# Kernel tuning notes

Measured on AMD Instinct MI355X. Metric: run time of the kernel, lower is better.

Reference implementation:

```python
import jax, jax.numpy as jnp
import numpy as np

THRESHOLD = 0.004  # graph_threshold from init_kwargs
EPS = 1e-12


def setup_inputs() -> dict:
    key = jax.random.key(0)
    kf, kw = jax.random.split(key)
    features = jax.random.normal(kf, (8192, 128), dtype=jnp.float32)
    weight = jax.random.normal(kw, (128, 128), dtype=jnp.float32)
    return {"features": features, "weight": weight}


def reference(features, weight):
    # Pairwise state fidelity: squared dot product of row-normalized vectors.
    n = features.shape[0]
    xn = features / (jnp.linalg.norm(features, axis=1, keepdims=True) + EPS)
    fid = (xn @ xn.T) ** 2  # [N, N]
    # Edge weight 1.0 where fid >= threshold (secondary=None); no self-loops.
    adj = (fid >= THRESHOLD).astype(features.dtype)
    adj = adj * (1.0 - jnp.eye(n, dtype=features.dtype))
    aggregated = adj @ features  # [N, F]
    # relu(W @ agg.T).T == relu(agg @ W.T)
    return jax.nn.relu(aggregated @ weight.T)
```

## Files before the change

### kernel.cpp

```cpp
#include <hip/hip_runtime.h>
#include <math.h>

#define NROWS 8192
#define NF    128
#define THRF  0.004f
#define BM    128
#define BN    64
#define QN    2048
#define NITER 32

typedef _Float16 f16;
typedef __attribute__((ext_vector_type(8))) _Float16 f16x8;
typedef __attribute__((ext_vector_type(4))) float f32x4;

#define MFMA16F(a, b, c) __builtin_amdgcn_mfma_f32_16x16x32_f16(a, b, c, 0, 0, 0)

#define RH_OFF 0
#define RL_OFF 32768
#define TB_OFF 65536
#define PB_OFF 98304
#define IJ_OFF 114688
#define SM_BYTES 115200

typedef __attribute__((address_space(1))) const unsigned int g_u32;
typedef __attribute__((address_space(3))) unsigned int l_u32;

__device__ __forceinline__ void gload16(const void* g, void* l) {
    __builtin_amdgcn_global_load_lds((g_u32*)g, (l_u32*)l, 16, 0, 0);
}

__device__ __forceinline__ unsigned short f16bits(f16 x) {
    return __builtin_bit_cast(unsigned short, x);
}

__global__ __launch_bounds__(256) void prep_k(const float* __restrict__ X,
                                              float* __restrict__ inv_norm,
                                              unsigned short* __restrict__ Xh,
                                              unsigned short* __restrict__ Xl,
                                              unsigned short* __restrict__ XhT) {
    __shared__ unsigned short sT[64][136];
    const int t  = threadIdx.x;
    const int jb = blockIdx.x * 64;
    const int row = t >> 2, c0 = (t & 3) * 32;
    const int grow = jb + row;

    float v[32];
    {
        const float* src = X + (size_t)grow * NF + c0;
        #pragma unroll
        for (int k = 0; k < 8; ++k) {
            f32x4 e = *reinterpret_cast<const f32x4*>(src + 4 * k);
            v[4 * k]     = e[0]; v[4 * k + 1] = e[1];
            v[4 * k + 2] = e[2]; v[4 * k + 3] = e[3];
        }
    }
    float ss = 0.f;
    #pragma unroll
    for (int k = 0; k < 32; ++k) ss += v[k] * v[k];
    ss += __shfl_xor(ss, 1);
    ss += __shfl_xor(ss, 2);
    if ((t & 3) == 0) inv_norm[grow] = 1.0f / (sqrtf(ss) + 1e-12f);

    #pragma unroll
    for (int k = 0; k < 4; ++k) {
        unsigned hw[4], lw[4];
        #pragma unroll
        for (int p = 0; p < 4; ++p) {
            float a = v[8 * k + 2 * p], b = v[8 * k + 2 * p + 1];
            f16 ha = (f16)a, hb = (f16)b;
            f16 la = (f16)((a - (float)ha) * 2048.0f);
            f16 lb = (f16)((b - (float)hb) * 2048.0f);
            hw[p] = (unsigned)f16bits(ha) | ((unsigned)f16bits(hb) << 16);
            lw[p] = (unsigned)f16bits(la) | ((unsigned)f16bits(lb) << 16);
        }
        uint4 h4 = {hw[0], hw[1], hw[2], hw[3]};
        uint4 l4 = {lw[0], lw[1], lw[2], lw[3]};
        *reinterpret_cast<uint4*>(Xh + (size_t)grow * NF + c0 + 8 * k) = h4;
        *reinterpret_cast<uint4*>(Xl + (size_t)grow * NF + c0 + 8 * k) = l4;
        unsigned* sp = reinterpret_cast<unsigned*>(&sT[row][c0 + 8 * k]);
        sp[0] = hw[0]; sp[1] = hw[1]; sp[2] = hw[2]; sp[3] = hw[3];
    }
    __syncthreads();
    {
        int f = t >> 1, qh = t & 1;
        unsigned um[16];
        #pragma unroll
        for (int m = 0; m < 16; ++m) {
            int j = 32 * qh + 2 * m;
            um[m] = (unsigned)sT[j][f] | ((unsigned)sT[j + 1][f] << 16);
        }
        unsigned* dst = reinterpret_cast<unsigned*>(XhT + (size_t)f * NROWS + jb + 32 * qh);
        #pragma unroll
        for (int m = 0; m < 16; ++m) dst[m] = um[m];
    }
}

__device__ __forceinline__ void issue_tiles(const unsigned short* __restrict__ Xh,
                                            const unsigned short* __restrict__ Xl,
                                            const unsigned short* __restrict__ XhT,
                                            char* SM, int w, int l, int jwin, int buf) {
    const int r16 = l >> 4, c16 = l & 15;
    #pragma unroll
    for (int u = 0; u < 2; ++u) {
        int jloc = 8 * w + 4 * u + r16;
        size_t src = (size_t)(jwin + jloc) * NF + ((c16 ^ (jloc & 15)) << 3);
        gload16(Xh + src, SM + RH_OFF + buf * 16384 + (8 * w + 4 * u) * 256);
        gload16(Xl + src, SM + RL_OFF + buf * 16384 + (8 * w + 4 * u) * 256);
    }
    const int r8 = l >> 3, c8 = l & 7;
    #pragma unroll
    for (int u = 0; u < 2; ++u) {
        int floc = 16 * w + 8 * u + r8;
        const unsigned short* src = XhT + (size_t)floc * NROWS + jwin + ((c8 ^ (floc & 7)) << 3);
        gload16(src, SM + TB_OFF + buf * 16384 + (16 * w + 8 * u) * 128);
    }
}

__global__ __launch_bounds__(512, 2) void fused_k(const unsigned short* __restrict__ Xh,
                                                  const unsigned short* __restrict__ Xl,
                                                  const unsigned short* __restrict__ XhT,
                                                  const float* __restrict__ inv_norm,
                                                  float* __restrict__ out) {
    __shared__ __align__(16) char SM[SM_BYTES];
    const int t = threadIdx.x;
    const int w = t >> 6, l = t & 63, l15 = l & 15, h = l >> 4;
    const int im2 = w >> 1;
    const int jn2 = w & 1;
    const int bid   = blockIdx.x;
    const int ibase = (bid >> 2) * BM;
    const int qbase = (bid & 3) * QN;

    f16x8 aH[2][4], aL[2][4];
    #pragma unroll
    for (int is = 0; is < 2; ++is) {
        const size_t ro = (size_t)(ibase + 32 * im2 + 16 * is + l15) * NF;
        #pragma unroll
        for (int ks = 0; ks < 4; ++ks) {
            aH[is][ks] = *reinterpret_cast<const f16x8*>(Xh + ro + 32 * ks + 8 * h);
            aL[is][ks] = *reinterpret_cast<const f16x8*>(Xl + ro + 32 * ks + 8 * h);
        }
    }
    float invI2[8];
    #pragma unroll
    for (int is = 0; is < 2; ++is)
        #pragma unroll
        for (int q = 0; q < 4; ++q) {
            float x = inv_norm[ibase + 32 * im2 + 16 * is + 4 * h + q];
            invI2[is * 4 + q] = x * x;
        }

    issue_tiles(Xh, Xl, XhT, SM, w, l, qbase, 0);
    if (t < BN) { float x = inv_norm[qbase + t]; ((float*)(SM + IJ_OFF))[t] = x * x; }

    f32x4 agg[2][4];
    #pragma unroll
    for (int is = 0; is < 2; ++is)
        #pragma unroll
        for (int fs = 0; fs < 4; ++fs)
            #pragma unroll
            for (int q = 0; q < 4; ++q) agg[is][fs][q] = 0.f;

    for (int it = 0; it < NITER; ++it) {
        const int buf  = it & 1;
        const int jwin = qbase + it * BN;
        __syncthreads();
        if (it + 1 < NITER) {
            issue_tiles(Xh, Xl, XhT, SM, w, l, jwin + BN, buf ^ 1);
            if (t < BN) {
                float x = inv_norm[jwin + BN + t];
                ((float*)(SM + IJ_OFF))[(buf ^ 1) * BN + t] = x * x;
            }
        }
        const char* rh = SM + RH_OFF + buf * 16384;
        const char* rl = SM + RL_OFF + buf * 16384;
        f32x4 Shi[2][2], Slo[2][2];
        #pragma unroll
        for (int js = 0; js < 2; ++js)
            #pragma unroll
            for (int is = 0; is < 2; ++is)
                #pragma unroll
                for (int q = 0; q < 4; ++q) { Shi[js][is][q] = 0.f; Slo[js][is][q] = 0.f; }
        __builtin_amdgcn_s_setprio(1);
        #pragma unroll
        for (int ks = 0; ks < 4; ++ks) {
            #pragma unroll
            for (int js = 0; js < 2; ++js) {
                int jl = 32 * jn2 + 16 * js + l15;
                int boff = jl * 256 + (((4 * ks + h) ^ (jl & 15)) << 4);
                f16x8 bh = *reinterpret_cast<const f16x8*>(rh + boff);
                f16x8 bl = *reinterpret_cast<const f16x8*>(rl + boff);
                #pragma unroll
                for (int is = 0; is < 2; ++is) {
                    Shi[js][is] = MFMA16F(aH[is][ks], bh, Shi[js][is]);
                    Slo[js][is] = MFMA16F(aL[is][ks], bh, Slo[js][is]);
                    Slo[js][is] = MFMA16F(aH[is][ks], bl, Slo[js][is]);
                }
            }
        }
        __builtin_amdgcn_s_setprio(0);

        #pragma unroll
        for (int js = 0; js < 2; ++js) {
            int jc = 32 * jn2 + 16 * js + l15;
            float ij2 = ((const float*)(SM + IJ_OFF))[buf * BN + jc];
            #pragma unroll
            for (int is = 0; is < 2; ++is) {
                int di = (jwin + jc) - (ibase + 32 * im2 + 16 * is + 4 * h);
                #pragma unroll
                for (int q = 0; q < 4; ++q) {
                    float vv = Shi[js][is][q] + Slo[js][is][q] * (1.0f / 2048.0f);
                    float t2 = vv * vv * invI2[is * 4 + q] * ij2;
                    bool p = (t2 >= THRF) && (di != q);
                    int il = 32 * im2 + 16 * is + 4 * h + q;
                    int pb = il * 128 + ((jc * 2) ^ ((il & 7) << 4));
                    *reinterpret_cast<unsigned short*>(SM + PB_OFF + pb) =
                        p ? (unsigned short)0x3C00 : (unsigned short)0;
                }
            }
        }
        asm volatile("s_waitcnt lgkmcnt(0)\n\ts_barrier" ::: "memory");

        const char* tbp = SM + TB_OFF + buf * 16384;
        __builtin_amdgcn_s_setprio(1);
        #pragma unroll
        for (int kj = 0; kj < 2; ++kj) {
            f16x8 pa[2];
            #pragma unroll
            for (int is = 0; is < 2; ++is) {
                int ir = 32 * im2 + 16 * is + l15;
                pa[is] = *reinterpret_cast<const f16x8*>(
                    SM + PB_OFF + ir * 128 + ((64 * kj + 16 * h) ^ ((ir & 7) << 4)));
            }
            #pragma unroll
            for (int fs = 0; fs < 4; ++fs) {
                int f = 64 * jn2 + 16 * fs + l15;
                f16x8 bt = *reinterpret_cast<const f16x8*>(
                    tbp + f * 128 + ((64 * kj + 16 * h) ^ ((f & 7) << 4)));
                agg[0][fs] = MFMA16F(pa[0], bt, agg[0][fs]);
                agg[1][fs] = MFMA16F(pa[1], bt, agg[1][fs]);
            }
        }
        __builtin_amdgcn_s_setprio(0);
    }

    #pragma unroll
    for (int is = 0; is < 2; ++is)
        #pragma unroll
        for (int fs = 0; fs < 4; ++fs) {
            int col = 64 * jn2 + 16 * fs + l15;
            #pragma unroll
            for (int q = 0; q < 4; ++q) {
                int row = ibase + 32 * im2 + 16 * is + 4 * h + q;
                atomicAdd(&out[(size_t)row * NF + col], agg[is][fs][q]);
            }
        }
}

__global__ __launch_bounds__(256) void combine_k(const float* __restrict__ Wm,
                                                 float* __restrict__ out) {
    __shared__ float sW[NF * NF];
    __shared__ float sSum[32][132];
    const int t = threadIdx.x;
    const size_t base = (size_t)blockIdx.x * 32 * NF;
    #pragma unroll
    for (int k = 0; k < 16; ++k) {
        int u4 = t + 256 * k;
        reinterpret_cast<f32x4*>(sW)[u4] = reinterpret_cast<const f32x4*>(Wm)[u4];
    }
    #pragma unroll
    for (int k = 0; k < 4; ++k) {
        int u4 = t + 256 * k;
        f32x4 v = reinterpret_cast<const f32x4*>(out + base)[u4];
        *reinterpret_cast<f32x4*>(&sSum[u4 >> 5][(4 * u4) & 127]) = v;
    }
    __syncthreads();
    const int r = t & 31, og = t >> 5;
    float acc[16];
    #pragma unroll
    for (int oi = 0; oi < 16; ++oi) acc[oi] = 0.f;
    #pragma unroll 8
    for (int k4 = 0; k4 < 32; ++k4) {
        f32x4 a4 = *reinterpret_cast<const f32x4*>(&sSum[r][4 * k4]);
        #pragma unroll
        for (int oi = 0; oi < 16; ++oi) {
            f32x4 w4 = *reinterpret_cast<const f32x4*>(&sW[(og * 16 + oi) * NF + 4 * k4]);
            acc[oi] += a4[0] * w4[0] + a4[1] * w4[1] + a4[2] * w4[2] + a4[3] * w4[3];
        }
    }
    #pragma unroll
    for (int o4 = 0; o4 < 4; ++o4) {
        f32x4 v4;
        #pragma unroll
        for (int e = 0; e < 4; ++e) {
            float v = acc[o4 * 4 + e];
            v4[e] = v > 0.f ? v : 0.f;
        }
        *reinterpret_cast<f32x4*>(out + base + r * NF + og * 16 + o4 * 4) = v4;
    }
}

extern "C" void kernel_launch(void* const* d_in, const int* in_sizes, int n_in,
                              void* d_out, int out_size, void* d_ws, size_t ws_size,
                              hipStream_t stream) {
    const float* feat = (const float*)d_in[0];
    const float* Wm   = (const float*)d_in[1];
    float* out        = (float*)d_out;

    char* ws = (char*)d_ws;
    unsigned short* Xh  = (unsigned short*)(ws);
    unsigned short* Xl  = (unsigned short*)(ws + (2u << 20));
    unsigned short* XhT = (unsigned short*)(ws + (4u << 20));
    float* inv_norm     = (float*)(ws + (6u << 20));

    hipMemsetAsync(out, 0, (size_t)out_size * sizeof(float), stream);
    prep_k<<<NROWS / 64, 256, 0, stream>>>(feat, inv_norm, Xh, Xl, XhT);
    fused_k<<<256, 512, 0, stream>>>(Xh, Xl, XhT, inv_norm, out);
    combine_k<<<NROWS / 32, 256, 0, stream>>>(Wm, out);
}
```

Before: 107.9 us.

## Remap warp tiling to 2x4 layout and replace memset with zero kernel

Warps are now arranged as 2 along rows by 4 along columns. Each warp covers 64 rows and 16 j-columns in the fidelity GEMM, so it loads each B fragment once and reuses it across 4 row subtiles, and it covers 32 feature columns in the aggregation GEMM. This cuts the LDS B reads in the first GEMM but doubles the A-fragment registers (aH/aL become 4x4), which raises register pressure at 2 blocks per CU. The hipMemsetAsync on the output is replaced by a small vectorized zeroing kernel to avoid memset overhead.

After: 126.1 us. +16.8%, slower.

```diff
diff --git a/kernel.cpp b/kernel.cpp
--- a/kernel.cpp
+++ b/kernel.cpp
@@ -31,6 +31,13 @@
 
 __device__ __forceinline__ unsigned short f16bits(f16 x) {
     return __builtin_bit_cast(unsigned short, x);
+}
+
+__global__ __launch_bounds__(256) void zero_k(float* __restrict__ out) {
+    int idx = blockIdx.x * 512 + threadIdx.x;
+    f32x4 z = {0.f, 0.f, 0.f, 0.f};
+    reinterpret_cast<f32x4*>(out)[idx]       = z;
+    reinterpret_cast<f32x4*>(out)[idx + 256] = z;
 }
 
 __global__ __launch_bounds__(256) void prep_k(const float* __restrict__ X,
@@ -124,41 +131,43 @@
     __shared__ __align__(16) char SM[SM_BYTES];
     const int t = threadIdx.x;
     const int w = t >> 6, l = t & 63, l15 = l & 15, h = l >> 4;
-    const int im2 = w >> 1;
-    const int jn2 = w & 1;
+    const int iw = w & 1;
+    const int jw = w >> 1;
     const int bid   = blockIdx.x;
     const int ibase = (bid >> 2) * BM;
     const int qbase = (bid & 3) * QN;
 
-    f16x8 aH[2][4], aL[2][4];
-    #pragma unroll
-    for (int is = 0; is < 2; ++is) {
-        const size_t ro = (size_t)(ibase + 32 * im2 + 16 * is + l15) * NF;
+    f16x8 aH[4][4], aL[4][4];
+    #pragma unroll
+    for (int is = 0; is < 4; ++is) {
+        const size_t ro = (size_t)(ibase + 64 * iw + 16 * is + l15) * NF;
         #pragma unroll
         for (int ks = 0; ks < 4; ++ks) {
             aH[is][ks] = *reinterpret_cast<const f16x8*>(Xh + ro + 32 * ks + 8 * h);
             aL[is][ks] = *reinterpret_cast<const f16x8*>(Xl + ro + 32 * ks + 8 * h);
         }
     }
-    float invI2[8];
-    #pragma unroll
-    for (int is = 0; is < 2; ++is)
+    float invI2[16];
+    #pragma unroll
+    for (int is = 0; is < 4; ++is)
         #pragma unroll
         for (int q = 0; q < 4; ++q) {
-            float x = inv_norm[ibase + 32 * im2 + 16 * is + 4 * h + q];
+            float x = inv_norm[ibase + 64 * iw + 16 * is + 4 * h + q];
             invI2[is * 4 + q] = x * x;
         }
 
     issue_tiles(Xh, Xl, XhT, SM, w, l, qbase, 0);
     if (t < BN) { float x = inv_norm[qbase + t]; ((float*)(SM + IJ_OFF))[t] = x * x; }
 
-    f32x4 agg[2][4];
-    #pragma unroll
-    for (int is = 0; is < 2; ++is)
-        #pragma unroll
-        for (int fs = 0; fs < 4; ++fs)
-            #pragma unroll
-            for (int q = 0; q < 4; ++q) agg[is][fs][q] = 0.f;
+    f32x4 agg[4][2];
+    #pragma unroll
+    for (int is = 0; is < 4; ++is)
+        #pragma unroll
+        for (int nf = 0; nf < 2; ++nf)
+            #pragma unroll
+            for (int q = 0; q < 4; ++q) agg[is][nf][q] = 0.f;
+
+    const int jl = 16 * jw + l15;
 
     for (int it = 0; it < NITER; ++it) {
         const int buf  = it & 1;
@@ -171,48 +180,42 @@
                 ((float*)(SM + IJ_OFF))[(buf ^ 1) * BN + t] = x * x;
             }
         }
-        const char* rh = SM + RH_OFF + buf * 16384;
-        const char* rl = SM + RL_OFF + buf * 16384;
-        f32x4 Shi[2][2], Slo[2][2];
-        #pragma unroll
-        for (int js = 0; js < 2; ++js)
-            #pragma unroll
-            for (int is = 0; is < 2; ++is)
-                #pragma unroll
-                for (int q = 0; q < 4; ++q) { Shi[js][is][q] = 0.f; Slo[js][is][q] = 0.f; }
+        const char* rh  = SM + RH_OFF + buf * 16384;
+        const char* rl  = SM + RL_OFF + buf * 16384;
+        const char* tbp = SM + TB_OFF + buf * 16384;
+
+        f32x4 Shi[4], Slo[4];
+        #pragma unroll
+        for (int is = 0; is < 4; ++is)
+            #pragma unroll
+            for (int q = 0; q < 4; ++q) { Shi[is][q] = 0.f; Slo[is][q] = 0.f; }
         __builtin_amdgcn_s_setprio(1);
         #pragma unroll
         for (int ks = 0; ks < 4; ++ks) {
-            #pragma unroll
-            for (int js = 0; js < 2; ++js) {
-                int jl = 32 * jn2 + 16 * js + l15;
-                int boff = jl * 256 + (((4 * ks + h) ^ (jl & 15)) << 4);
-                f16x8 bh = *reinterpret_cast<const f16x8*>(rh + boff);
-                f16x8 bl = *reinterpret_cast<const f16x8*>(rl + boff);
-                #pragma unroll
-                for (int is = 0; is < 2; ++is) {
-                    Shi[js][is] = MFMA16F(aH[is][ks], bh, Shi[js][is]);
-                    Slo[js][is] = MFMA16F(aL[is][ks], bh, Slo[js][is]);
-                    Slo[js][is] = MFMA16F(aH[is][ks], bl, Slo[js][is]);
-                }
+            int boff = jl * 256 + (((4 * ks + h) ^ (jl & 15)) << 4);
+            f16x8 bh = *reinterpret_cast<const f16x8*>(rh + boff);
+            f16x8 bl = *reinterpret_cast<const f16x8*>(rl + boff);
+            #pragma unroll
+            for (int is = 0; is < 4; ++is) {
+                Shi[is] = MFMA16F(aH[is][ks], bh, Shi[is]);
+                Slo[is] = MFMA16F(aL[is][ks], bh, Slo[is]);
+                Slo[is] = MFMA16F(aH[is][ks], bl, Slo[is]);
             }
         }
         __builtin_amdgcn_s_setprio(0);
 
-        #pragma unroll
-        for (int js = 0; js < 2; ++js) {
-            int jc = 32 * jn2 + 16 * js + l15;
-            float ij2 = ((const float*)(SM + IJ_OFF))[buf * BN + jc];
-            #pragma unroll
-            for (int is = 0; is < 2; ++is) {
-                int di = (jwin + jc) - (ibase + 32 * im2 + 16 * is + 4 * h);
+        {
+            float ij2 = ((const float*)(SM + IJ_OFF))[buf * BN + jl];
+            #pragma unroll
+            for (int is = 0; is < 4; ++is) {
+                int di = (jwin + jl) - (ibase + 64 * iw + 16 * is + 4 * h);
                 #pragma unroll
                 for (int q = 0; q < 4; ++q) {
-                    float vv = Shi[js][is][q] + Slo[js][is][q] * (1.0f / 2048.0f);
+                    float vv = Shi[is][q] + Slo[is][q] * (1.0f / 2048.0f);
                     float t2 = vv * vv * invI2[is * 4 + q] * ij2;
                     bool p = (t2 >= THRF) && (di != q);
-                    int il = 32 * im2 + 16 * is + 4 * h + q;
-                    int pb = il * 128 + ((jc * 2) ^ ((il & 7) << 4));
+                    int il = 64 * iw + 16 * is + 4 * h + q;
+                    int pb = il * 128 + ((jl * 2) ^ ((il & 7) << 4));
                     *reinterpret_cast<unsigned short*>(SM + PB_OFF + pb) =
                         p ? (unsigned short)0x3C00 : (unsigned short)0;
                 }
@@ -220,38 +223,37 @@
         }
         asm volatile("s_waitcnt lgkmcnt(0)\n\ts_barrier" ::: "memory");
 
-        const char* tbp = SM + TB_OFF + buf * 16384;
         __builtin_amdgcn_s_setprio(1);
         #pragma unroll
         for (int kj = 0; kj < 2; ++kj) {
-            f16x8 pa[2];
-            #pragma unroll
-            for (int is = 0; is < 2; ++is) {
-                int ir = 32 * im2 + 16 * is + l15;
-                pa[is] = *reinterpret_cast<const f16x8*>(
+            f16x8 bt[2];
+            #pragma unroll
+            for (int nf = 0; nf < 2; ++nf) {
+                int f = 32 * jw + 16 * nf + l15;
+                bt[nf] = *reinterpret_cast<const f16x8*>(
+                    tbp + f * 128 + ((64 * kj + 16 * h) ^ ((f & 7) << 4)));
+            }
+            #pragma unroll
+            for (int is = 0; is < 4; ++is) {
+                int ir = 64 * iw + 16 * is + l15;
+                f16x8 pa = *reinterpret_cast<const f16x8*>(
                     SM + PB_OFF + ir * 128 + ((64 * kj + 16 * h) ^ ((ir & 7) << 4)));
-            }
-            #pragma unroll
-            for (int fs = 0; fs < 4; ++fs) {
-                int f = 64 * jn2 + 16 * fs + l15;
-                f16x8 bt = *reinterpret_cast<const f16x8*>(
-                    tbp + f * 128 + ((64 * kj + 16 * h) ^ ((f & 7) << 4)));
-                agg[0][fs] = MFMA16F(pa[0], bt, agg[0][fs]);
-                agg[1][fs] = MFMA16F(pa[1], bt, agg[1][fs]);
+                agg[is][0] = MFMA16F(pa, bt[0], agg[is][0]);
+                agg[is][1] = MFMA16F(pa, bt[1], agg[is][1]);
             }
         }
         __builtin_amdgcn_s_setprio(0);
     }
 
     #pragma unroll
-    for (int is = 0; is < 2; ++is)
-        #pragma unroll
-        for (int fs = 0; fs < 4; ++fs) {
-            int col = 64 * jn2 + 16 * fs + l15;
+    for (int is = 0; is < 4; ++is)
+        #pragma unroll
+        for (int nf = 0; nf < 2; ++nf) {
+            int col = 32 * jw + 16 * nf + l15;
             #pragma unroll
             for (int q = 0; q < 4; ++q) {
-                int row = ibase + 32 * im2 + 16 * is + 4 * h + q;
-                atomicAdd(&out[(size_t)row * NF + col], agg[is][fs][q]);
+                int row = ibase + 64 * iw + 16 * is + 4 * h + q;
+                atomicAdd(&out[(size_t)row * NF + col], agg[is][nf][q]);
             }
         }
 }
@@ -312,7 +314,7 @@
     unsigned short* XhT = (unsigned short*)(ws + (4u << 20));
     float* inv_norm     = (float*)(ws + (6u << 20));
 
-    hipMemsetAsync(out, 0, (size_t)out_size * sizeof(float), stream);
+    zero_k<<<NROWS * NF / 2048, 256, 0, stream>>>(out);
     prep_k<<<NROWS / 64, 256, 0, stream>>>(feat, inv_norm, Xh, Xl, XhT);
     fused_k<<<256, 512, 0, stream>>>(Xh, Xl, XhT, inv_norm, out);
     combine_k<<<NROWS / 32, 256, 0, stream>>>(Wm, out);
```

## Halve column tile and split work over twice as many blocks for occupancy

Applied to the files above, without the earlier changes.

Shrinks the per-iteration column window from 64 to 32 and the per-block column range from 2048 to 1024, so the fused kernel launches 512 blocks with half the LDS and an occupancy hint of 4 blocks per CU. Tile loading, the swizzles and the predicate buffer layout are reworked for the smaller tiles. The aim is more resident waves and better latency hiding on 256 CUs, at the cost of twice as many global atomic adds to the output and more barriers per unit of work. It also replaces hipMemsetAsync with a small zeroing kernel.

Result: slower. 180.6 us (+67.3%).

```diff
diff --git a/kernel.cpp b/kernel.cpp
--- a/kernel.cpp
+++ b/kernel.cpp
@@ -5,8 +5,8 @@
 #define NF    128
 #define THRF  0.004f
 #define BM    128
-#define BN    64
-#define QN    2048
+#define BN    32
+#define QN    1024
 #define NITER 32
 
 typedef _Float16 f16;
@@ -16,11 +16,11 @@
 #define MFMA16F(a, b, c) __builtin_amdgcn_mfma_f32_16x16x32_f16(a, b, c, 0, 0, 0)
 
 #define RH_OFF 0
-#define RL_OFF 32768
-#define TB_OFF 65536
-#define PB_OFF 98304
-#define IJ_OFF 114688
-#define SM_BYTES 115200
+#define RL_OFF 16384
+#define TB_OFF 32768
+#define PB_OFF 49152
+#define IJ_OFF 57344
+#define SM_BYTES 57600
 
 typedef __attribute__((address_space(1))) const unsigned int g_u32;
 typedef __attribute__((address_space(3))) unsigned int l_u32;
@@ -31,6 +31,13 @@
 
 __device__ __forceinline__ unsigned short f16bits(f16 x) {
     return __builtin_bit_cast(unsigned short, x);
+}
+
+__global__ __launch_bounds__(256) void zero_k(float* __restrict__ out) {
+    int idx = blockIdx.x * 512 + threadIdx.x;
+    f32x4 z = {0.f, 0.f, 0.f, 0.f};
+    reinterpret_cast<f32x4*>(out)[idx]       = z;
+    reinterpret_cast<f32x4*>(out)[idx + 256] = z;
 }
 
 __global__ __launch_bounds__(256) void prep_k(const float* __restrict__ X,
@@ -99,24 +106,18 @@
                                             const unsigned short* __restrict__ Xl,
                                             const unsigned short* __restrict__ XhT,
                                             char* SM, int w, int l, int jwin, int buf) {
-    const int r16 = l >> 4, c16 = l & 15;
-    #pragma unroll
-    for (int u = 0; u < 2; ++u) {
-        int jloc = 8 * w + 4 * u + r16;
-        size_t src = (size_t)(jwin + jloc) * NF + ((c16 ^ (jloc & 15)) << 3);
-        gload16(Xh + src, SM + RH_OFF + buf * 16384 + (8 * w + 4 * u) * 256);
-        gload16(Xl + src, SM + RL_OFF + buf * 16384 + (8 * w + 4 * u) * 256);
-    }
-    const int r8 = l >> 3, c8 = l & 7;
-    #pragma unroll
-    for (int u = 0; u < 2; ++u) {
-        int floc = 16 * w + 8 * u + r8;
-        const unsigned short* src = XhT + (size_t)floc * NROWS + jwin + ((c8 ^ (floc & 7)) << 3);
-        gload16(src, SM + TB_OFF + buf * 16384 + (16 * w + 8 * u) * 128);
-    }
-}
-
-__global__ __launch_bounds__(512, 2) void fused_k(const unsigned short* __restrict__ Xh,
+    const int jr = 4 * w + (l >> 4), c16 = l & 15;
+    size_t src = (size_t)(jwin + jr) * NF + ((c16 ^ (jr & 15)) << 3);
+    gload16(Xh + src, SM + RH_OFF + buf * 8192 + 4 * w * 256);
+    gload16(Xl + src, SM + RL_OFF + buf * 8192 + 4 * w * 256);
+
+    const int f = 16 * w + (l >> 2), c4 = l & 3;
+    const unsigned short* tsrc = XhT + (size_t)f * NROWS + jwin +
+                                 ((c4 ^ ((f ^ (f >> 2)) & 3)) << 3);
+    gload16(tsrc, SM + TB_OFF + buf * 8192 + 16 * w * 64);
+}
+
+__global__ __launch_bounds__(512, 4) void fused_k(const unsigned short* __restrict__ Xh,
                                                   const unsigned short* __restrict__ Xl,
                                                   const unsigned short* __restrict__ XhT,
                                                   const float* __restrict__ inv_norm,
@@ -124,16 +125,16 @@
     __shared__ __align__(16) char SM[SM_BYTES];
     const int t = threadIdx.x;
     const int w = t >> 6, l = t & 63, l15 = l & 15, h = l >> 4;
-    const int im2 = w >> 1;
-    const int jn2 = w & 1;
+    const int im = w >> 1;
+    const int jn = w & 1;
     const int bid   = blockIdx.x;
-    const int ibase = (bid >> 2) * BM;
-    const int qbase = (bid & 3) * QN;
+    const int ibase = (bid >> 3) * BM;
+    const int qbase = (bid & 7) * QN;
 
     f16x8 aH[2][4], aL[2][4];
     #pragma unroll
     for (int is = 0; is < 2; ++is) {
-        const size_t ro = (size_t)(ibase + 32 * im2 + 16 * is + l15) * NF;
+        const size_t ro = (size_t)(ibase + 32 * im + 16 * is + l15) * NF;
         #pragma unroll
         for (int ks = 0; ks < 4; ++ks) {
             aH[is][ks] = *reinterpret_cast<const f16x8*>(Xh + ro + 32 * ks + 8 * h);
@@ -145,7 +146,7 @@
     for (int is = 0; is < 2; ++is)
         #pragma unroll
         for (int q = 0; q < 4; ++q) {
-            float x = inv_norm[ibase + 32 * im2 + 16 * is + 4 * h + q];
+            float x = inv_norm[ibase + 32 * im + 16 * is + 4 * h + q];
             invI2[is * 4 + q] = x * x;
         }
 
@@ -159,6 +160,8 @@
         for (int fs = 0; fs < 4; ++fs)
             #pragma unroll
             for (int q = 0; q < 4; ++q) agg[is][fs][q] = 0.f;
+
+    const int jl = 16 * jn + l15;
 
     for (int it = 0; it < NITER; ++it) {
         const int buf  = it & 1;
@@ -171,48 +174,42 @@
                 ((float*)(SM + IJ_OFF))[(buf ^ 1) * BN + t] = x * x;
             }
         }
-        const char* rh = SM + RH_OFF + buf * 16384;
-        const char* rl = SM + RL_OFF + buf * 16384;
-        f32x4 Shi[2][2], Slo[2][2];
-        #pragma unroll
-        for (int js = 0; js < 2; ++js)
-            #pragma unroll
-            for (int is = 0; is < 2; ++is)
-                #pragma unroll
-                for (int q = 0; q < 4; ++q) { Shi[js][is][q] = 0.f; Slo[js][is][q] = 0.f; }
+        const char* rh  = SM + RH_OFF + buf * 8192;
+        const char* rl  = SM + RL_OFF + buf * 8192;
+        const char* tbp = SM + TB_OFF + buf * 8192;
+
+        f32x4 Shi[2], Slo[2];
+        #pragma unroll
+        for (int is = 0; is < 2; ++is)
+            #pragma unroll
+            for (int q = 0; q < 4; ++q) { Shi[is][q] = 0.f; Slo[is][q] = 0.f; }
         __builtin_amdgcn_s_setprio(1);
         #pragma unroll
         for (int ks = 0; ks < 4; ++ks) {
-            #pragma unroll
-            for (int js = 0; js < 2; ++js) {
-                int jl = 32 * jn2 + 16 * js + l15;
-                int boff = jl * 256 + (((4 * ks + h) ^ (jl & 15)) << 4);
-                f16x8 bh = *reinterpret_cast<const f16x8*>(rh + boff);
-                f16x8 bl = *reinterpret_cast<const f16x8*>(rl + boff);
-                #pragma unroll
-                for (int is = 0; is < 2; ++is) {
-                    Shi[js][is] = MFMA16F(aH[is][ks], bh, Shi[js][is]);
-                    Slo[js][is] = MFMA16F(aL[is][ks], bh, Slo[js][is]);
-                    Slo[js][is] = MFMA16F(aH[is][ks], bl, Slo[js][is]);
-                }
+            int boff = jl * 256 + (((4 * ks + h) ^ (jl & 15)) << 4);
+            f16x8 bh = *reinterpret_cast<const f16x8*>(rh + boff);
+            f16x8 bl = *reinterpret_cast<const f16x8*>(rl + boff);
+            #pragma unroll
+            for (int is = 0; is < 2; ++is) {
+                Shi[is] = MFMA16F(aH[is][ks], bh, Shi[is]);
+                Slo[is] = MFMA16F(aL[is][ks], bh, Slo[is]);
+                Slo[is] = MFMA16F(aH[is][ks], bl, Slo[is]);
             }
         }
         __builtin_amdgcn_s_setprio(0);
 
-        #pragma unroll
-        for (int js = 0; js < 2; ++js) {
-            int jc = 32 * jn2 + 16 * js + l15;
-            float ij2 = ((const float*)(SM + IJ_OFF))[buf * BN + jc];
+        {
+            float ij2 = ((const float*)(SM + IJ_OFF))[buf * BN + jl];
             #pragma unroll
             for (int is = 0; is < 2; ++is) {
-                int di = (jwin + jc) - (ibase + 32 * im2 + 16 * is + 4 * h);
+                int di = (jwin + jl) - (ibase + 32 * im + 16 * is + 4 * h);
                 #pragma unroll
                 for (int q = 0; q < 4; ++q) {
-                    float vv = Shi[js][is][q] + Slo[js][is][q] * (1.0f / 2048.0f);
+                    float vv = Shi[is][q] + Slo[is][q] * (1.0f / 2048.0f);
                     float t2 = vv * vv * invI2[is * 4 + q] * ij2;
                     bool p = (t2 >= THRF) && (di != q);
-                    int il = 32 * im2 + 16 * is + 4 * h + q;
-                    int pb = il * 128 + ((jc * 2) ^ ((il & 7) << 4));
+                    int il = 32 * im + 16 * is + 4 * h + q;
+                    int pb = il * 64 + ((jl * 2) ^ (((il ^ (il >> 2)) & 3) << 4));
                     *reinterpret_cast<unsigned short*>(SM + PB_OFF + pb) =
                         p ? (unsigned short)0x3C00 : (unsigned short)0;
                 }
@@ -220,22 +217,20 @@
         }
         asm volatile("s_waitcnt lgkmcnt(0)\n\ts_barrier" ::: "memory");
 
-        const char* tbp = SM + TB_OFF + buf * 16384;
         __builtin_amdgcn_s_setprio(1);
-        #pragma unroll
-        for (int kj = 0; kj < 2; ++kj) {
+        {
             f16x8 pa[2];
             #pragma unroll
             for (int is = 0; is < 2; ++is) {
-                int ir = 32 * im2 + 16 * is + l15;
+                int ir = 32 * im + 16 * is + l15;
                 pa[is] = *reinterpret_cast<const f16x8*>(
-                    SM + PB_OFF + ir * 128 + ((64 * kj + 16 * h) ^ ((ir & 7) << 4)));
+                    SM + PB_OFF + ir * 64 + ((16 * h) ^ (((ir ^ (ir >> 2)) & 3) << 4)));
             }
             #pragma unroll
             for (int fs = 0; fs < 4; ++fs) {
-                int f = 64 * jn2 + 16 * fs + l15;
+                int f = 64 * jn + 16 * fs + l15;
                 f16x8 bt = *reinterpret_cast<const f16x8*>(
-                    tbp + f * 128 + ((64 * kj + 16 * h) ^ ((f & 7) << 4)));
+                    tbp + f * 64 + ((16 * h) ^ (((f ^ (f >> 2)) & 3) << 4)));
                 agg[0][fs] = MFMA16F(pa[0], bt, agg[0][fs]);
                 agg[1][fs] = MFMA16F(pa[1], bt, agg[1][fs]);
             }
@@ -247,10 +242,10 @@
     for (int is = 0; is < 2; ++is)
         #pragma unroll
         for (int fs = 0; fs < 4; ++fs) {
-            int col = 64 * jn2 + 16 * fs + l15;
+            int col = 64 * jn + 16 * fs + l15;
             #pragma unroll
             for (int q = 0; q < 4; ++q) {
-                int row = ibase + 32 * im2 + 16 * is + 4 * h + q;
+                int row = ibase + 32 * im + 16 * is + 4 * h + q;
                 atomicAdd(&out[(size_t)row * NF + col], agg[is][fs][q]);
             }
         }
@@ -312,8 +307,8 @@
     unsigned short* XhT = (unsigned short*)(ws + (4u << 20));
     float* inv_norm     = (float*)(ws + (6u << 20));
 
-    hipMemsetAsync(out, 0, (size_t)out_size * sizeof(float), stream);
+    zero_k<<<NROWS * NF / 2048, 256, 0, stream>>>(out);
     prep_k<<<NROWS / 64, 256, 0, stream>>>(feat, inv_norm, Xh, Xl, XhT);
-    fused_k<<<256, 512, 0, stream>>>(Xh, Xl, XhT, inv_norm, out);
+    fused_k<<<512, 512, 0, stream>>>(Xh, Xl, XhT, inv_norm, out);
     combine_k<<<NROWS / 32, 256, 0, stream>>>(Wm, out);
 }
```

## Load low-half B operands directly from global, shrink LDS, replace memset kernel

Applied to the files above, without the earlier changes.

The low-precision correction tile (Xl) is no longer staged through LDS. Each lane now reads its B fragments straight from global memory into registers, and the per-column inverse norms are read from global instead of an LDS array. This cuts LDS footprint and the async copy traffic per iteration, which may help occupancy and LDS bandwidth, at the cost of exposed global-load latency inside the MFMA loop. hipMemsetAsync is replaced by a small custom zeroing kernel, and empty asm barriers pin the A fragments in VGPRs.

Measured after the change: 145.5 us. 34.8% more time.

```diff
diff --git a/kernel.cpp b/kernel.cpp
--- a/kernel.cpp
+++ b/kernel.cpp
@@ -16,11 +16,9 @@
 #define MFMA16F(a, b, c) __builtin_amdgcn_mfma_f32_16x16x32_f16(a, b, c, 0, 0, 0)
 
 #define RH_OFF 0
-#define RL_OFF 32768
-#define TB_OFF 65536
-#define PB_OFF 98304
-#define IJ_OFF 114688
-#define SM_BYTES 115200
+#define TB_OFF 32768
+#define PB_OFF 65536
+#define SM_BYTES 81920
 
 typedef __attribute__((address_space(1))) const unsigned int g_u32;
 typedef __attribute__((address_space(3))) unsigned int l_u32;
@@ -31,6 +29,13 @@
 
 __device__ __forceinline__ unsigned short f16bits(f16 x) {
     return __builtin_bit_cast(unsigned short, x);
+}
+
+__global__ __launch_bounds__(256) void zero_k(float* __restrict__ out) {
+    int idx = blockIdx.x * 512 + threadIdx.x;
+    f32x4 z = {0.f, 0.f, 0.f, 0.f};
+    reinterpret_cast<f32x4*>(out)[idx]       = z;
+    reinterpret_cast<f32x4*>(out)[idx + 256] = z;
 }
 
 __global__ __launch_bounds__(256) void prep_k(const float* __restrict__ X,
@@ -96,7 +101,6 @@
 }
 
 __device__ __forceinline__ void issue_tiles(const unsigned short* __restrict__ Xh,
-                                            const unsigned short* __restrict__ Xl,
                                             const unsigned short* __restrict__ XhT,
                                             char* SM, int w, int l, int jwin, int buf) {
     const int r16 = l >> 4, c16 = l & 15;
@@ -105,7 +109,6 @@
         int jloc = 8 * w + 4 * u + r16;
         size_t src = (size_t)(jwin + jloc) * NF + ((c16 ^ (jloc & 15)) << 3);
         gload16(Xh + src, SM + RH_OFF + buf * 16384 + (8 * w + 4 * u) * 256);
-        gload16(Xl + src, SM + RL_OFF + buf * 16384 + (8 * w + 4 * u) * 256);
     }
     const int r8 = l >> 3, c8 = l & 7;
     #pragma unroll
@@ -140,6 +143,13 @@
             aL[is][ks] = *reinterpret_cast<const f16x8*>(Xl + ro + 32 * ks + 8 * h);
         }
     }
+    #pragma unroll
+    for (int is = 0; is < 2; ++is)
+        #pragma unroll
+        for (int ks = 0; ks < 4; ++ks) {
+            asm volatile("" : "+v"(aH[is][ks]));
+            asm volatile("" : "+v"(aL[is][ks]));
+        }
     float invI2[8];
     #pragma unroll
     for (int is = 0; is < 2; ++is)
@@ -149,8 +159,7 @@
             invI2[is * 4 + q] = x * x;
         }
 
-    issue_tiles(Xh, Xl, XhT, SM, w, l, qbase, 0);
-    if (t < BN) { float x = inv_norm[qbase + t]; ((float*)(SM + IJ_OFF))[t] = x * x; }
+    issue_tiles(Xh, XhT, SM, w, l, qbase, 0);
 
     f32x4 agg[2][4];
     #pragma unroll
@@ -164,45 +173,51 @@
         const int buf  = it & 1;
         const int jwin = qbase + it * BN;
         __syncthreads();
-        if (it + 1 < NITER) {
-            issue_tiles(Xh, Xl, XhT, SM, w, l, jwin + BN, buf ^ 1);
-            if (t < BN) {
-                float x = inv_norm[jwin + BN + t];
-                ((float*)(SM + IJ_OFF))[(buf ^ 1) * BN + t] = x * x;
-            }
-        }
-        const char* rh = SM + RH_OFF + buf * 16384;
-        const char* rl = SM + RL_OFF + buf * 16384;
+        if (it + 1 < NITER) issue_tiles(Xh, XhT, SM, w, l, jwin + BN, buf ^ 1);
+
+        const char* rh  = SM + RH_OFF + buf * 16384;
+        const char* tbp = SM + TB_OFF + buf * 16384;
+
+        float jn0, jn1;
+        {
+            int jc0 = 32 * jn2 + l15, jc1 = jc0 + 16;
+            jn0 = inv_norm[jwin + jc0];
+            jn1 = inv_norm[jwin + jc1];
+        }
+
         f32x4 Shi[2][2], Slo[2][2];
         #pragma unroll
-        for (int js = 0; js < 2; ++js)
+        for (int js = 0; js < 2; ++js) {
+            const int jl = 32 * jn2 + 16 * js + l15;
+            const unsigned short* xlr = Xl + (size_t)(jwin + jl) * NF + 8 * h;
+            f16x8 blg[4];
+            #pragma unroll
+            for (int ks = 0; ks < 4; ++ks)
+                blg[ks] = *reinterpret_cast<const f16x8*>(xlr + 32 * ks);
             #pragma unroll
             for (int is = 0; is < 2; ++is)
                 #pragma unroll
                 for (int q = 0; q < 4; ++q) { Shi[js][is][q] = 0.f; Slo[js][is][q] = 0.f; }
-        __builtin_amdgcn_s_setprio(1);
-        #pragma unroll
-        for (int ks = 0; ks < 4; ++ks) {
-            #pragma unroll
-            for (int js = 0; js < 2; ++js) {
-                int jl = 32 * jn2 + 16 * js + l15;
+            __builtin_amdgcn_s_setprio(1);
+            #pragma unroll
+            for (int ks = 0; ks < 4; ++ks) {
                 int boff = jl * 256 + (((4 * ks + h) ^ (jl & 15)) << 4);
                 f16x8 bh = *reinterpret_cast<const f16x8*>(rh + boff);
-                f16x8 bl = *reinterpret_cast<const f16x8*>(rl + boff);
                 #pragma unroll
                 for (int is = 0; is < 2; ++is) {
                     Shi[js][is] = MFMA16F(aH[is][ks], bh, Shi[js][is]);
                     Slo[js][is] = MFMA16F(aL[is][ks], bh, Slo[js][is]);
-                    Slo[js][is] = MFMA16F(aH[is][ks], bl, Slo[js][is]);
+                    Slo[js][is] = MFMA16F(aH[is][ks], blg[ks], Slo[js][is]);
                 }
             }
-        }
-        __builtin_amdgcn_s_setprio(0);
+            __builtin_amdgcn_s_setprio(0);
+        }
 
         #pragma unroll
         for (int js = 0; js < 2; ++js) {
             int jc = 32 * jn2 + 16 * js + l15;
-            float ij2 = ((const float*)(SM + IJ_OFF))[buf * BN + jc];
+            float xj = js ? jn1 : jn0;
+            float ij2 = xj * xj;
             #pragma unroll
             for (int is = 0; is < 2; ++is) {
                 int di = (jwin + jc) - (ibase + 32 * im2 + 16 * is + 4 * h);
@@ -220,7 +235,6 @@
         }
         asm volatile("s_waitcnt lgkmcnt(0)\n\ts_barrier" ::: "memory");
 
-        const char* tbp = SM + TB_OFF + buf * 16384;
         __builtin_amdgcn_s_setprio(1);
         #pragma unroll
         for (int kj = 0; kj < 2; ++kj) {
@@ -312,7 +326,7 @@
     unsigned short* XhT = (unsigned short*)(ws + (4u << 20));
     float* inv_norm     = (float*)(ws + (6u << 20));
 
-    hipMemsetAsync(out, 0, (size_t)out_size * sizeof(float), stream);
+    zero_k<<<NROWS * NF / 2048, 256, 0, stream>>>(out);
     prep_k<<<NROWS / 64, 256, 0, stream>>>(feat, inv_norm, Xh, Xl, XhT);
     fused_k<<<256, 512, 0, stream>>>(Xh, Xl, XhT, inv_norm, out);
     combine_k<<<NROWS / 32, 256, 0, stream>>>(Wm, out);
```
